# Kernel optimization log

Hardware: AMD Instinct MI355X
Metric: run time of the kernel (lower is better)

## Reference

```python
import jax, jax.numpy as jnp
import numpy as np


def setup_inputs() -> dict:
    key = jax.random.key(0)
    ks = jax.random.split(key, 8)
    b, s1, s2 = 16, 512, 40
    video_dim, text_dim, attn_dim = 1024, 300, 256
    return {
        "video": jax.random.normal(ks[0], (b, s1, video_dim), dtype=jnp.float32),
        "text": jax.random.normal(ks[1], (b, s2, text_dim), dtype=jnp.float32),
        "w1": jax.random.normal(ks[2], (video_dim, attn_dim), dtype=jnp.float32),
        "w2": jax.random.normal(ks[3], (text_dim, attn_dim), dtype=jnp.float32),
        "w3": jax.random.normal(ks[4], (attn_dim, 1), dtype=jnp.float32),
        "bias": jax.random.normal(ks[5], (attn_dim,), dtype=jnp.float32),
        "w4": jax.random.normal(ks[6], (4 * attn_dim, 500), dtype=jnp.float32),
        "b4": jax.random.normal(ks[7], (500,), dtype=jnp.float32),
    }


def reference(video, text, w1, w2, w3, bias, w4, b4):
    # video: (b, s1, d1), text: (b, s2, d2)
    e = jnp.einsum("bsd,da->bsa", video, w1)   # (b, s1, a) -- also 'hh' in original
    f = jnp.einsum("btd,da->bta", text, w2)    # (b, s2, a)
    # additive attention energies: tanh over (b, s1, s2, a) broadcast sum
    h = jnp.tanh(e[:, :, None, :] + f[:, None, :, :] + bias)  # (b, s1, s2, a)
    logits = jnp.squeeze(jnp.einsum("bsta,ao->bsto", h, w3), -1)  # (b, s1, s2)
    # original expands logits over attn_dim then softmaxes dim=2; identical to
    # softmax over s2 of the scalar scores, broadcast afterwards.
    attn = jax.nn.softmax(logits, axis=2)  # (b, s1, s2)
    text_attn = jnp.einsum("bst,bta->bsa", attn, f)  # (b, s1, a)
    cont = jnp.concatenate(
        [e, text_attn, e * text_attn, e - text_attn], axis=-1
    )  # (b, s1, 4a)
    return jnp.tanh(cont) @ w4 + b4  # (b, s1, 500)
```

## Files before the change

### kernel.cpp

```cpp
#include <hip/hip_runtime.h>
#include <hip/hip_bf16.h>
#include <cstdint>

typedef __attribute__((ext_vector_type(8))) short bf16x8;
typedef __attribute__((ext_vector_type(4))) short bf16x4;
typedef __attribute__((ext_vector_type(4))) float f32x4;

#define TANH_SCALE 2.8853900817779268f
#define TANH_UNSCALE 0.34657359027997264f

__device__ __forceinline__ short cvt_bf16(float f) {
  union { float f; uint32_t u; } x; x.f = f;
  uint32_t r = x.u + 0x7FFFu + ((x.u >> 16) & 1u);
  return (short)(r >> 16);
}
__device__ __forceinline__ float bf16_to_f(short s) {
  union { uint32_t u; float f; } x; x.u = ((uint32_t)(uint16_t)s) << 16;
  return x.f;
}

__device__ __forceinline__ float tanh_fast(float x) {
  float e = __builtin_amdgcn_exp2f(x * TANH_SCALE);
  return 1.0f - 2.0f * __builtin_amdgcn_rcpf(e + 1.0f);
}
__device__ __forceinline__ float tanh_pre(float xs) {
  float e = __builtin_amdgcn_exp2f(xs);
  return 1.0f - 2.0f * __builtin_amdgcn_rcpf(e + 1.0f);
}

__global__ __launch_bounds__(256) void k_prep(const float* __restrict__ video,
                                              const float* __restrict__ text,
                                              const float* __restrict__ w1,
                                              const float* __restrict__ w2,
                                              const float* __restrict__ w4,
                                              short* __restrict__ vhi,
                                              short* __restrict__ vlo,
                                              short* __restrict__ w1h,
                                              short* __restrict__ w1l,
                                              short* __restrict__ w4T,
                                              short* __restrict__ th,
                                              short* __restrict__ tl,
                                              short* __restrict__ w2h,
                                              short* __restrict__ w2l) {
  __shared__ float tile[32][33];
  int bid = blockIdx.x;
  if (bid < 1024) {
    int i = bid * 256 + threadIdx.x;
    for (; i < 2097152; i += 1024 * 256) {
      float4 v = ((const float4*)video)[i];
      bf16x4 h, l;
      h.x = cvt_bf16(v.x); h.y = cvt_bf16(v.y); h.z = cvt_bf16(v.z); h.w = cvt_bf16(v.w);
      l.x = cvt_bf16(v.x - bf16_to_f(h.x));
      l.y = cvt_bf16(v.y - bf16_to_f(h.y));
      l.z = cvt_bf16(v.z - bf16_to_f(h.z));
      l.w = cvt_bf16(v.w - bf16_to_f(h.w));
      ((bf16x4*)vhi)[i] = h;
      ((bf16x4*)vlo)[i] = l;
    }
  } else if (bid < 1280) {
    int idx = bid - 1024;
    int r0 = (idx & 31) * 32, c0 = (idx >> 5) * 32;
    int j = threadIdx.x & 31, i0 = threadIdx.x >> 5;
    #pragma unroll
    for (int i = i0; i < 32; i += 8) tile[i][j] = w1[(size_t)(r0 + i) * 256 + c0 + j];
    __syncthreads();
    #pragma unroll
    for (int i = i0; i < 32; i += 8) {
      float v = tile[j][i];
      short h = cvt_bf16(v);
      w1h[(size_t)(c0 + i) * 1024 + r0 + j] = h;
      w1l[(size_t)(c0 + i) * 1024 + r0 + j] = cvt_bf16(v - bf16_to_f(h));
    }
  } else if (bid < 1792) {
    int idx = bid - 1280;
    int r0 = (idx & 31) * 32, c0 = (idx >> 5) * 32;
    int j = threadIdx.x & 31, i0 = threadIdx.x >> 5;
    #pragma unroll
    for (int i = i0; i < 32; i += 8) {
      int c = c0 + j;
      tile[i][j] = (c < 500) ? w4[(size_t)(r0 + i) * 500 + c] : 0.f;
    }
    __syncthreads();
    #pragma unroll
    for (int i = i0; i < 32; i += 8)
      w4T[(size_t)(c0 + i) * 1024 + r0 + j] = cvt_bf16(tile[j][i]);
  } else if (bid < 1952) {
    int idx = bid - 1792;
    int row = idx * 4 + (threadIdx.x >> 6);
    int cl = threadIdx.x & 63;
    const float* trow = text + (size_t)row * 300;
    short* hrow = th + (size_t)row * 320;
    short* lrow = tl + (size_t)row * 320;
    #pragma unroll
    for (int c0 = 0; c0 < 320; c0 += 64) {
      int c = c0 + cl;
      float v = (c < 300) ? trow[c] : 0.f;
      short h = cvt_bf16(v);
      hrow[c] = h;
      lrow[c] = cvt_bf16(v - bf16_to_f(h));
    }
  } else {
    int idx = bid - 1952;
    int rt = idx % 10, ct = idx / 10;
    int r0 = rt * 32, c0 = ct * 32;
    int j = threadIdx.x & 31, i0 = threadIdx.x >> 5;
    #pragma unroll
    for (int i = i0; i < 32; i += 8) {
      int r = r0 + i;
      tile[i][j] = (r < 300) ? w2[(size_t)r * 256 + c0 + j] : 0.f;
    }
    __syncthreads();
    #pragma unroll
    for (int i = i0; i < 32; i += 8) {
      float v = tile[j][i];
      short h = cvt_bf16(v);
      w2h[(size_t)(c0 + i) * 320 + r0 + j] = h;
      w2l[(size_t)(c0 + i) * 320 + r0 + j] = cvt_bf16(v - bf16_to_f(h));
    }
  }
}

__global__ __launch_bounds__(256) void k_gemm_split(const short* __restrict__ Ah,
                                                    const short* __restrict__ Al,
                                                    const short* __restrict__ BTh,
                                                    const short* __restrict__ BTl,
                                                    float* __restrict__ C,
                                                    int K, int ldc) {
  __shared__ __align__(16) short Ash[64][72];
  __shared__ __align__(16) short Asl[64][72];
  __shared__ __align__(16) short Bsh[64][72];
  __shared__ __align__(16) short Bsl[64][72];
  int m0 = blockIdx.x * 64, n0 = blockIdx.y * 64;
  int tid = threadIdx.x, lane = tid & 63, wave = tid >> 6;
  int wm = (wave & 1) * 32, wn = (wave >> 1) * 32;
  int srow = tid >> 3, sseg = (tid & 7) * 8;
  f32x4 acc[2][2];
  #pragma unroll
  for (int i = 0; i < 2; i++)
    #pragma unroll
    for (int j = 0; j < 2; j++) acc[i][j] = (f32x4){0.f, 0.f, 0.f, 0.f};
  int mrow = lane & 15, quad = lane >> 4;

  for (int k0 = 0; k0 < K; k0 += 64) {
    size_t aoff0 = (size_t)(m0 + srow) * K + k0 + sseg;
    size_t aoff1 = aoff0 + (size_t)32 * K;
    size_t boff0 = (size_t)(n0 + srow) * K + k0 + sseg;
    size_t boff1 = boff0 + (size_t)32 * K;
    bf16x8 a0h = *(const bf16x8*)(Ah + aoff0);
    bf16x8 a1h = *(const bf16x8*)(Ah + aoff1);
    bf16x8 a0l = *(const bf16x8*)(Al + aoff0);
    bf16x8 a1l = *(const bf16x8*)(Al + aoff1);
    bf16x8 b0h = *(const bf16x8*)(BTh + boff0);
    bf16x8 b1h = *(const bf16x8*)(BTh + boff1);
    bf16x8 b0l = *(const bf16x8*)(BTl + boff0);
    bf16x8 b1l = *(const bf16x8*)(BTl + boff1);
    __syncthreads();
    *(bf16x8*)&Ash[srow][sseg] = a0h;  *(bf16x8*)&Ash[srow + 32][sseg] = a1h;
    *(bf16x8*)&Asl[srow][sseg] = a0l;  *(bf16x8*)&Asl[srow + 32][sseg] = a1l;
    *(bf16x8*)&Bsh[srow][sseg] = b0h;  *(bf16x8*)&Bsh[srow + 32][sseg] = b1h;
    *(bf16x8*)&Bsl[srow][sseg] = b0l;  *(bf16x8*)&Bsl[srow + 32][sseg] = b1l;
    __syncthreads();
    #pragma unroll
    for (int ks = 0; ks < 2; ks++) {
      int kk = ks * 32 + quad * 8;
      bf16x8 ah[2], al[2], bh[2], bl[2];
      ah[0] = *(const bf16x8*)&Ash[wm + mrow][kk];
      ah[1] = *(const bf16x8*)&Ash[wm + 16 + mrow][kk];
      al[0] = *(const bf16x8*)&Asl[wm + mrow][kk];
      al[1] = *(const bf16x8*)&Asl[wm + 16 + mrow][kk];
      bh[0] = *(const bf16x8*)&Bsh[wn + mrow][kk];
      bh[1] = *(const bf16x8*)&Bsh[wn + 16 + mrow][kk];
      bl[0] = *(const bf16x8*)&Bsl[wn + mrow][kk];
      bl[1] = *(const bf16x8*)&Bsl[wn + 16 + mrow][kk];
      #pragma unroll
      for (int i = 0; i < 2; i++)
        #pragma unroll
        for (int j = 0; j < 2; j++) {
          acc[i][j] = __builtin_amdgcn_mfma_f32_16x16x32_bf16(ah[i], bh[j], acc[i][j], 0, 0, 0);
          acc[i][j] = __builtin_amdgcn_mfma_f32_16x16x32_bf16(ah[i], bl[j], acc[i][j], 0, 0, 0);
          acc[i][j] = __builtin_amdgcn_mfma_f32_16x16x32_bf16(al[i], bh[j], acc[i][j], 0, 0, 0);
        }
    }
  }
  int rbase = quad * 4;
  #pragma unroll
  for (int i = 0; i < 2; i++)
    #pragma unroll
    for (int j = 0; j < 2; j++) {
      int col = n0 + wn + j * 16 + mrow;
      #pragma unroll
      for (int r = 0; r < 4; r++) {
        int row = m0 + wm + i * 16 + rbase + r;
        C[(size_t)row * ldc + col] = acc[i][j][r];
      }
    }
}

__device__ __forceinline__ void load_lds16(void* lds, const void* g) {
  __builtin_amdgcn_global_load_lds(
      (const __attribute__((address_space(1))) void*)g,
      (__attribute__((address_space(3))) void*)lds, 16, 0, 0);
}

__global__ __launch_bounds__(256) void k_gemm_e2(const short* __restrict__ Ah,
                                                 const short* __restrict__ Al,
                                                 const short* __restrict__ BTh,
                                                 const short* __restrict__ BTl,
                                                 float* __restrict__ Cparts,
                                                 int K, int ldc) {
  __shared__ __align__(16) short Ash[128][64];
  __shared__ __align__(16) short Asl[128][64];
  __shared__ __align__(16) short Bsh[64][64];
  __shared__ __align__(16) short Bsl[64][64];
  int m0 = blockIdx.x * 128, n0 = blockIdx.y * 64;
  int kz0 = blockIdx.z * 512;
  int tid = threadIdx.x, lane = tid & 63, wave = tid >> 6;
  int wm = wave * 32;
  int mrow = lane & 15, quad = lane >> 4;
  int lrow = lane >> 3, lseg = (lane & 7) * 8;

  f32x4 acc[2][4];
  #pragma unroll
  for (int i = 0; i < 2; i++)
    #pragma unroll
    for (int j = 0; j < 4; j++) acc[i][j] = (f32x4){0.f, 0.f, 0.f, 0.f};

  for (int k0 = kz0; k0 < kz0 + 512; k0 += 64) {
    __syncthreads();
    #pragma unroll
    for (int i = 0; i < 4; i++) {
      int c = wave * 4 + i;
      size_t go = (size_t)(m0 + c * 8 + lrow) * K + k0 + lseg;
      load_lds16(&Ash[c * 8][0], Ah + go);
      load_lds16(&Asl[c * 8][0], Al + go);
    }
    #pragma unroll
    for (int i = 0; i < 2; i++) {
      int c = wave * 2 + i;
      size_t go = (size_t)(n0 + c * 8 + lrow) * K + k0 + lseg;
      load_lds16(&Bsh[c * 8][0], BTh + go);
      load_lds16(&Bsl[c * 8][0], BTl + go);
    }
    __syncthreads();
    #pragma unroll
    for (int ks = 0; ks < 2; ks++) {
      int kk = ks * 32 + quad * 8;
      bf16x8 ah[2], al[2], bh[4], bl[4];
      #pragma unroll
      for (int i = 0; i < 2; i++) {
        ah[i] = *(const bf16x8*)&Ash[wm + i * 16 + mrow][kk];
        al[i] = *(const bf16x8*)&Asl[wm + i * 16 + mrow][kk];
      }
      #pragma unroll
      for (int j = 0; j < 4; j++) {
        bh[j] = *(const bf16x8*)&Bsh[j * 16 + mrow][kk];
        bl[j] = *(const bf16x8*)&Bsl[j * 16 + mrow][kk];
      }
      #pragma unroll
      for (int i = 0; i < 2; i++)
        #pragma unroll
        for (int j = 0; j < 4; j++) {
          acc[i][j] = __builtin_amdgcn_mfma_f32_16x16x32_bf16(ah[i], bh[j], acc[i][j], 0, 0, 0);
          acc[i][j] = __builtin_amdgcn_mfma_f32_16x16x32_bf16(ah[i], bl[j], acc[i][j], 0, 0, 0);
          acc[i][j] = __builtin_amdgcn_mfma_f32_16x16x32_bf16(al[i], bh[j], acc[i][j], 0, 0, 0);
        }
    }
  }
  float* C = Cparts + (size_t)blockIdx.z * 8192 * 256;
  int rbase = quad * 4;
  #pragma unroll
  for (int i = 0; i < 2; i++)
    #pragma unroll
    for (int j = 0; j < 4; j++) {
      int col = n0 + j * 16 + mrow;
      #pragma unroll
      for (int r = 0; r < 4; r++) {
        int row = m0 + wm + i * 16 + rbase + r;
        C[(size_t)row * ldc + col] = acc[i][j][r];
      }
    }
}

__global__ __launch_bounds__(256) void k_gemm_f(const short* __restrict__ A,
                                                const short* __restrict__ BT,
                                                const float* __restrict__ bias,
                                                float* __restrict__ C,
                                                int K, int ldc, int nstore) {
  __shared__ __align__(16) short As[128][64];
  __shared__ __align__(16) short Bs[64][64];
  int m0 = blockIdx.x * 128, n0 = blockIdx.y * 64;
  int tid = threadIdx.x, lane = tid & 63, wave = tid >> 6;
  int wm = wave * 32;
  int mrow = lane & 15, quad = lane >> 4;
  int lrow = lane >> 3, lseg = (lane & 7) * 8;

  f32x4 acc[2][4];
  #pragma unroll
  for (int i = 0; i < 2; i++)
    #pragma unroll
    for (int j = 0; j < 4; j++) acc[i][j] = (f32x4){0.f, 0.f, 0.f, 0.f};

  for (int k0 = 0; k0 < K; k0 += 64) {
    __syncthreads();
    #pragma unroll
    for (int i = 0; i < 4; i++) {
      int c = wave * 4 + i;
      load_lds16(&As[c * 8][0], A + (size_t)(m0 + c * 8 + lrow) * K + k0 + lseg);
    }
    #pragma unroll
    for (int i = 0; i < 2; i++) {
      int c = wave * 2 + i;
      load_lds16(&Bs[c * 8][0], BT + (size_t)(n0 + c * 8 + lrow) * K + k0 + lseg);
    }
    __syncthreads();
    #pragma unroll
    for (int ks = 0; ks < 2; ks++) {
      int kk = ks * 32 + quad * 8;
      bf16x8 af[2], bf[4];
      #pragma unroll
      for (int i = 0; i < 2; i++) af[i] = *(const bf16x8*)&As[wm + i * 16 + mrow][kk];
      #pragma unroll
      for (int j = 0; j < 4; j++) bf[j] = *(const bf16x8*)&Bs[j * 16 + mrow][kk];
      #pragma unroll
      for (int i = 0; i < 2; i++)
        #pragma unroll
        for (int j = 0; j < 4; j++)
          acc[i][j] = __builtin_amdgcn_mfma_f32_16x16x32_bf16(af[i], bf[j], acc[i][j], 0, 0, 0);
    }
  }
  int rbase = quad * 4;
  #pragma unroll
  for (int i = 0; i < 2; i++)
    #pragma unroll
    for (int j = 0; j < 4; j++) {
      int col = n0 + j * 16 + mrow;
      if (col < nstore) {
        float bv = bias[col];
        #pragma unroll
        for (int r = 0; r < 4; r++) {
          int row = m0 + wm + i * 16 + rbase + r;
          C[(size_t)row * ldc + col] = acc[i][j][r] + bv;
        }
      }
    }
}

__global__ __launch_bounds__(512) void k_middle(const float* __restrict__ e0p,
                                                const float* __restrict__ e1p,
                                                const float* __restrict__ fb,
                                                const float* __restrict__ w3,
                                                const float* __restrict__ bias,
                                                short* __restrict__ cont) {
  __shared__ __align__(16) float fbs[40 * 256];
  __shared__ float lg[16][40];
  __shared__ float attn[16][40];
  int tid = threadIdx.x, wave = tid >> 6, lane = tid & 63;
  int la = lane & 31, half = lane >> 5;
  int row0 = blockIdx.x * 16;
  int b = row0 >> 9;
  int lgrow = wave + (half ? 8 : 0);
  int myrow = row0 + lgrow;

  const float4* fsrc = (const float4*)(fb + (size_t)b * 40 * 256);
  const float4* bias4 = (const float4*)bias;
  for (int i = tid; i < 40 * 64; i += 512) {
    float4 v = fsrc[i];
    float4 bb = bias4[i & 63];
    v.x = (v.x + bb.x) * TANH_SCALE; v.y = (v.y + bb.y) * TANH_SCALE;
    v.z = (v.z + bb.z) * TANH_SCALE; v.w = (v.w + bb.w) * TANH_SCALE;
    ((float4*)fbs)[i] = v;
  }
  __syncthreads();

  int a0 = la * 8;
  size_t eoff = (size_t)myrow * 256 + a0;
  float4 p00 = *(const float4*)(e0p + eoff);
  float4 p01 = *(const float4*)(e0p + eoff + 4);
  float4 p10 = *(const float4*)(e1p + eoff);
  float4 p11 = *(const float4*)(e1p + eoff + 4);
  float4 e0, e1;
  e0.x = p00.x + p10.x; e0.y = p00.y + p10.y; e0.z = p00.z + p10.z; e0.w = p00.w + p10.w;
  e1.x = p01.x + p11.x; e1.y = p01.y + p11.y; e1.z = p01.z + p11.z; e1.w = p01.w + p11.w;
  float4 w30 = *(const float4*)(w3 + a0);
  float4 w31 = *(const float4*)(w3 + a0 + 4);
  float4 bv0 = *(const float4*)(bias + a0);
  float4 bv1 = *(const float4*)(bias + a0 + 4);
  float4 es0, es1;
  es0.x = e0.x * TANH_SCALE; es0.y = e0.y * TANH_SCALE;
  es0.z = e0.z * TANH_SCALE; es0.w = e0.w * TANH_SCALE;
  es1.x = e1.x * TANH_SCALE; es1.y = e1.y * TANH_SCALE;
  es1.z = e1.z * TANH_SCALE; es1.w = e1.w * TANH_SCALE;

  for (int tc = 0; tc < 40; tc += 4) {
    float p[4];
    #pragma unroll
    for (int u = 0; u < 4; u++) {
      const float* fr = &fbs[(tc + u) * 256 + a0];
      float4 f0 = *(const float4*)fr;
      float4 f1 = *(const float4*)(fr + 4);
      p[u] = tanh_pre(es0.x + f0.x) * w30.x + tanh_pre(es0.y + f0.y) * w30.y
           + tanh_pre(es0.z + f0.z) * w30.z + tanh_pre(es0.w + f0.w) * w30.w
           + tanh_pre(es1.x + f1.x) * w31.x + tanh_pre(es1.y + f1.y) * w31.y
           + tanh_pre(es1.z + f1.z) * w31.z + tanh_pre(es1.w + f1.w) * w31.w;
    }
    #pragma unroll
    for (int s = 16; s >= 1; s >>= 1) {
      #pragma unroll
      for (int u = 0; u < 4; u++) p[u] += __shfl_xor(p[u], s, 64);
    }
    if (la == 0) {
      #pragma unroll
      for (int u = 0; u < 4; u++) lg[lgrow][tc + u] = p[u];
    }
  }

  auto softmax_row = [&](int r) {
    float x = (lane < 40) ? lg[r][lane] : -3.0e38f;
    float m = x;
    #pragma unroll
    for (int s = 32; s >= 1; s >>= 1) m = fmaxf(m, __shfl_xor(m, s, 64));
    float ex = (lane < 40) ? __builtin_amdgcn_exp2f((x - m) * 1.4426950408889634f) : 0.f;
    float ssum = ex;
    #pragma unroll
    for (int s = 32; s >= 1; s >>= 1) ssum += __shfl_xor(ssum, s, 64);
    if (lane < 40) attn[r][lane] = ex * __builtin_amdgcn_rcpf(ssum);
  };
  softmax_row(wave);
  softmax_row(wave + 8);

  float ac[8] = {0.f,0.f,0.f,0.f,0.f,0.f,0.f,0.f};
  for (int t = 0; t < 40; t++) {
    float w = attn[lgrow][t];
    const float* fr = &fbs[t * 256 + a0];
    float4 f0 = *(const float4*)fr;
    float4 f1 = *(const float4*)(fr + 4);
    ac[0] += w * f0.x; ac[1] += w * f0.y; ac[2] += w * f0.z; ac[3] += w * f0.w;
    ac[4] += w * f1.x; ac[5] += w * f1.y; ac[6] += w * f1.z; ac[7] += w * f1.w;
  }
  float tx[8];
  tx[0] = ac[0] * TANH_UNSCALE - bv0.x; tx[1] = ac[1] * TANH_UNSCALE - bv0.y;
  tx[2] = ac[2] * TANH_UNSCALE - bv0.z; tx[3] = ac[3] * TANH_UNSCALE - bv0.w;
  tx[4] = ac[4] * TANH_UNSCALE - bv1.x; tx[5] = ac[5] * TANH_UNSCALE - bv1.y;
  tx[6] = ac[6] * TANH_UNSCALE - bv1.z; tx[7] = ac[7] * TANH_UNSCALE - bv1.w;
  float ev[8] = {e0.x, e0.y, e0.z, e0.w, e1.x, e1.y, e1.z, e1.w};

  short* crow = cont + (size_t)myrow * 1024 + a0;
  auto st8 = [&](int off, const float* v) {
    bf16x8 pk;
    #pragma unroll
    for (int i = 0; i < 8; i++) pk[i] = cvt_bf16(v[i]);
    *(bf16x8*)(crow + off) = pk;
  };
  float s0[8], s1[8], s2[8], s3[8];
  #pragma unroll
  for (int i = 0; i < 8; i++) {
    s0[i] = tanh_fast(ev[i]);
    s1[i] = tanh_fast(tx[i]);
    s2[i] = tanh_fast(ev[i] * tx[i]);
    s3[i] = tanh_fast(ev[i] - tx[i]);
  }
  st8(0, s0); st8(256, s1); st8(512, s2); st8(768, s3);
}

extern "C" void kernel_launch(void* const* d_in, const int* in_sizes, int n_in,
                              void* d_out, int out_size, void* d_ws, size_t ws_size,
                              hipStream_t stream) {
  const float* video = (const float*)d_in[0];
  const float* text  = (const float*)d_in[1];
  const float* w1    = (const float*)d_in[2];
  const float* w2    = (const float*)d_in[3];
  const float* w3    = (const float*)d_in[4];
  const float* bias  = (const float*)d_in[5];
  const float* w4    = (const float*)d_in[6];
  const float* b4    = (const float*)d_in[7];
  float* out = (float*)d_out;
  char* ws = (char*)d_ws;

  short* video_hi = (short*)(ws);
  short* video_lo = (short*)(ws + 16777216);
  short* contbuf  = (short*)(ws + 16777216);
  short* w1T_hi   = (short*)(ws + 33554432);
  short* w1T_lo   = (short*)(ws + 34078720);
  short* w4T      = (short*)(ws + 34603008);
  float* fbuf     = (float*)(ws + 35651584);
  float* eparts   = (float*)(ws + 36306944);
  float* epart1   = (float*)(ws + 36306944 + 8388608);
  short* text_hi  = (short*)(ws + 36306944);
  short* text_lo  = (short*)(ws + 36306944 + 409600);
  short* w2T_hi   = (short*)(ws + 36306944 + 819200);
  short* w2T_lo   = (short*)(ws + 36306944 + 1024000);

  k_prep<<<2032, 256, 0, stream>>>(video, text, w1, w2, w4,
                                   video_hi, video_lo, w1T_hi, w1T_lo, w4T,
                                   text_hi, text_lo, w2T_hi, w2T_lo);
  k_gemm_split<<<dim3(10, 4), 256, 0, stream>>>(text_hi, text_lo, w2T_hi, w2T_lo,
                                                fbuf, 320, 256);
  k_gemm_e2<<<dim3(64, 4, 2), 256, 0, stream>>>(video_hi, video_lo, w1T_hi, w1T_lo,
                                                eparts, 1024, 256);
  k_middle<<<512, 512, 0, stream>>>(eparts, epart1, fbuf, w3, bias, contbuf);
  k_gemm_f<<<dim3(64, 8), 256, 0, stream>>>(contbuf, w4T, b4, out, 1024, 500, 500);
}
```

Measured before the change: 174.6 us.

## Fuse video bf16 split into e-GEMM and merge text GEMM into one launch

Result: faster. 164.6 us (-5.7%).

```diff
diff --git a/kernel.cpp b/kernel.cpp
--- a/kernel.cpp
+++ b/kernel.cpp
@@ -23,18 +23,35 @@
   float e = __builtin_amdgcn_exp2f(x * TANH_SCALE);
   return 1.0f - 2.0f * __builtin_amdgcn_rcpf(e + 1.0f);
 }
-__device__ __forceinline__ float tanh_pre(float xs) {
+__device__ __forceinline__ float sig_pre(float xs) {
   float e = __builtin_amdgcn_exp2f(xs);
-  return 1.0f - 2.0f * __builtin_amdgcn_rcpf(e + 1.0f);
-}
-
-__global__ __launch_bounds__(256) void k_prep(const float* __restrict__ video,
-                                              const float* __restrict__ text,
+  return __builtin_amdgcn_rcpf(e + 1.0f);
+}
+
+__device__ __forceinline__ void split8(float4 a, float4 b, bf16x8& h, bf16x8& l) {
+  float fa[8] = {a.x, a.y, a.z, a.w, b.x, b.y, b.z, b.w};
+  uint32_t uh[8], ul[8];
+  #pragma unroll
+  for (int j = 0; j < 8; j++) {
+    union { float f; uint32_t u; } x; x.f = fa[j];
+    uh[j] = x.u;
+    union { uint32_t u; float f; } t; t.u = x.u & 0xffff0000u;
+    union { float f; uint32_t u; } y; y.f = fa[j] - t.f;
+    ul[j] = y.u;
+  }
+  union { uint32_t w[4]; bf16x8 v; } H, L;
+  #pragma unroll
+  for (int j = 0; j < 4; j++) {
+    H.w[j] = __builtin_amdgcn_perm(uh[2 * j + 1], uh[2 * j], 0x07060302u);
+    L.w[j] = __builtin_amdgcn_perm(ul[2 * j + 1], ul[2 * j], 0x07060302u);
+  }
+  h = H.v; l = L.v;
+}
+
+__global__ __launch_bounds__(256) void k_prep(const float* __restrict__ text,
                                               const float* __restrict__ w1,
                                               const float* __restrict__ w2,
                                               const float* __restrict__ w4,
-                                              short* __restrict__ vhi,
-                                              short* __restrict__ vlo,
                                               short* __restrict__ w1h,
                                               short* __restrict__ w1l,
                                               short* __restrict__ w4T,
@@ -44,21 +61,8 @@
                                               short* __restrict__ w2l) {
   __shared__ float tile[32][33];
   int bid = blockIdx.x;
-  if (bid < 1024) {
-    int i = bid * 256 + threadIdx.x;
-    for (; i < 2097152; i += 1024 * 256) {
-      float4 v = ((const float4*)video)[i];
-      bf16x4 h, l;
-      h.x = cvt_bf16(v.x); h.y = cvt_bf16(v.y); h.z = cvt_bf16(v.z); h.w = cvt_bf16(v.w);
-      l.x = cvt_bf16(v.x - bf16_to_f(h.x));
-      l.y = cvt_bf16(v.y - bf16_to_f(h.y));
-      l.z = cvt_bf16(v.z - bf16_to_f(h.z));
-      l.w = cvt_bf16(v.w - bf16_to_f(h.w));
-      ((bf16x4*)vhi)[i] = h;
-      ((bf16x4*)vlo)[i] = l;
-    }
-  } else if (bid < 1280) {
-    int idx = bid - 1024;
+  if (bid < 256) {
+    int idx = bid;
     int r0 = (idx & 31) * 32, c0 = (idx >> 5) * 32;
     int j = threadIdx.x & 31, i0 = threadIdx.x >> 5;
     #pragma unroll
@@ -71,8 +75,8 @@
       w1h[(size_t)(c0 + i) * 1024 + r0 + j] = h;
       w1l[(size_t)(c0 + i) * 1024 + r0 + j] = cvt_bf16(v - bf16_to_f(h));
     }
-  } else if (bid < 1792) {
-    int idx = bid - 1280;
+  } else if (bid < 768) {
+    int idx = bid - 256;
     int r0 = (idx & 31) * 32, c0 = (idx >> 5) * 32;
     int j = threadIdx.x & 31, i0 = threadIdx.x >> 5;
     #pragma unroll
@@ -84,8 +88,8 @@
     #pragma unroll
     for (int i = i0; i < 32; i += 8)
       w4T[(size_t)(c0 + i) * 1024 + r0 + j] = cvt_bf16(tile[j][i]);
-  } else if (bid < 1952) {
-    int idx = bid - 1792;
+  } else if (bid < 928) {
+    int idx = bid - 768;
     int row = idx * 4 + (threadIdx.x >> 6);
     int cl = threadIdx.x & 63;
     const float* trow = text + (size_t)row * 300;
@@ -100,7 +104,7 @@
       lrow[c] = cvt_bf16(v - bf16_to_f(h));
     }
   } else {
-    int idx = bid - 1952;
+    int idx = bid - 928;
     int rt = idx % 10, ct = idx / 10;
     int r0 = rt * 32, c0 = ct * 32;
     int j = threadIdx.x & 31, i0 = threadIdx.x >> 5;
@@ -120,165 +124,186 @@
   }
 }
 
-__global__ __launch_bounds__(256) void k_gemm_split(const short* __restrict__ Ah,
-                                                    const short* __restrict__ Al,
-                                                    const short* __restrict__ BTh,
-                                                    const short* __restrict__ BTl,
-                                                    float* __restrict__ C,
-                                                    int K, int ldc) {
-  __shared__ __align__(16) short Ash[64][72];
-  __shared__ __align__(16) short Asl[64][72];
-  __shared__ __align__(16) short Bsh[64][72];
-  __shared__ __align__(16) short Bsl[64][72];
-  int m0 = blockIdx.x * 64, n0 = blockIdx.y * 64;
-  int tid = threadIdx.x, lane = tid & 63, wave = tid >> 6;
-  int wm = (wave & 1) * 32, wn = (wave >> 1) * 32;
-  int srow = tid >> 3, sseg = (tid & 7) * 8;
-  f32x4 acc[2][2];
-  #pragma unroll
-  for (int i = 0; i < 2; i++)
-    #pragma unroll
-    for (int j = 0; j < 2; j++) acc[i][j] = (f32x4){0.f, 0.f, 0.f, 0.f};
-  int mrow = lane & 15, quad = lane >> 4;
-
-  for (int k0 = 0; k0 < K; k0 += 64) {
-    size_t aoff0 = (size_t)(m0 + srow) * K + k0 + sseg;
-    size_t aoff1 = aoff0 + (size_t)32 * K;
-    size_t boff0 = (size_t)(n0 + srow) * K + k0 + sseg;
-    size_t boff1 = boff0 + (size_t)32 * K;
-    bf16x8 a0h = *(const bf16x8*)(Ah + aoff0);
-    bf16x8 a1h = *(const bf16x8*)(Ah + aoff1);
-    bf16x8 a0l = *(const bf16x8*)(Al + aoff0);
-    bf16x8 a1l = *(const bf16x8*)(Al + aoff1);
-    bf16x8 b0h = *(const bf16x8*)(BTh + boff0);
-    bf16x8 b1h = *(const bf16x8*)(BTh + boff1);
-    bf16x8 b0l = *(const bf16x8*)(BTl + boff0);
-    bf16x8 b1l = *(const bf16x8*)(BTl + boff1);
-    __syncthreads();
-    *(bf16x8*)&Ash[srow][sseg] = a0h;  *(bf16x8*)&Ash[srow + 32][sseg] = a1h;
-    *(bf16x8*)&Asl[srow][sseg] = a0l;  *(bf16x8*)&Asl[srow + 32][sseg] = a1l;
-    *(bf16x8*)&Bsh[srow][sseg] = b0h;  *(bf16x8*)&Bsh[srow + 32][sseg] = b1h;
-    *(bf16x8*)&Bsl[srow][sseg] = b0l;  *(bf16x8*)&Bsl[srow + 32][sseg] = b1l;
-    __syncthreads();
-    #pragma unroll
-    for (int ks = 0; ks < 2; ks++) {
-      int kk = ks * 32 + quad * 8;
-      bf16x8 ah[2], al[2], bh[2], bl[2];
-      ah[0] = *(const bf16x8*)&Ash[wm + mrow][kk];
-      ah[1] = *(const bf16x8*)&Ash[wm + 16 + mrow][kk];
-      al[0] = *(const bf16x8*)&Asl[wm + mrow][kk];
-      al[1] = *(const bf16x8*)&Asl[wm + 16 + mrow][kk];
-      bh[0] = *(const bf16x8*)&Bsh[wn + mrow][kk];
-      bh[1] = *(const bf16x8*)&Bsh[wn + 16 + mrow][kk];
-      bl[0] = *(const bf16x8*)&Bsl[wn + mrow][kk];
-      bl[1] = *(const bf16x8*)&Bsl[wn + 16 + mrow][kk];
-      #pragma unroll
-      for (int i = 0; i < 2; i++)
-        #pragma unroll
-        for (int j = 0; j < 2; j++) {
-          acc[i][j] = __builtin_amdgcn_mfma_f32_16x16x32_bf16(ah[i], bh[j], acc[i][j], 0, 0, 0);
-          acc[i][j] = __builtin_amdgcn_mfma_f32_16x16x32_bf16(ah[i], bl[j], acc[i][j], 0, 0, 0);
-          acc[i][j] = __builtin_amdgcn_mfma_f32_16x16x32_bf16(al[i], bh[j], acc[i][j], 0, 0, 0);
-        }
-    }
-  }
-  int rbase = quad * 4;
-  #pragma unroll
-  for (int i = 0; i < 2; i++)
-    #pragma unroll
-    for (int j = 0; j < 2; j++) {
-      int col = n0 + wn + j * 16 + mrow;
-      #pragma unroll
-      for (int r = 0; r < 4; r++) {
-        int row = m0 + wm + i * 16 + rbase + r;
-        C[(size_t)row * ldc + col] = acc[i][j][r];
-      }
-    }
-}
-
 __device__ __forceinline__ void load_lds16(void* lds, const void* g) {
   __builtin_amdgcn_global_load_lds(
       (const __attribute__((address_space(1))) void*)g,
       (__attribute__((address_space(3))) void*)lds, 16, 0, 0);
 }
 
-__global__ __launch_bounds__(256) void k_gemm_e2(const short* __restrict__ Ah,
-                                                 const short* __restrict__ Al,
-                                                 const short* __restrict__ BTh,
-                                                 const short* __restrict__ BTl,
-                                                 float* __restrict__ Cparts,
-                                                 int K, int ldc) {
-  __shared__ __align__(16) short Ash[128][64];
-  __shared__ __align__(16) short Asl[128][64];
-  __shared__ __align__(16) short Bsh[64][64];
-  __shared__ __align__(16) short Bsl[64][64];
-  int m0 = blockIdx.x * 128, n0 = blockIdx.y * 64;
-  int kz0 = blockIdx.z * 512;
+__global__ __launch_bounds__(256) void k_gemm_big(const float* __restrict__ video,
+                                                  const short* __restrict__ w1h,
+                                                  const short* __restrict__ w1l,
+                                                  const short* __restrict__ th,
+                                                  const short* __restrict__ tl,
+                                                  const short* __restrict__ w2h,
+                                                  const short* __restrict__ w2l,
+                                                  float* __restrict__ eparts,
+                                                  float* __restrict__ fbuf) {
+  __shared__ __align__(16) char smem[49152];
+  int bid = blockIdx.x;
   int tid = threadIdx.x, lane = tid & 63, wave = tid >> 6;
-  int wm = wave * 32;
   int mrow = lane & 15, quad = lane >> 4;
-  int lrow = lane >> 3, lseg = (lane & 7) * 8;
-
-  f32x4 acc[2][4];
-  #pragma unroll
-  for (int i = 0; i < 2; i++)
-    #pragma unroll
-    for (int j = 0; j < 4; j++) acc[i][j] = (f32x4){0.f, 0.f, 0.f, 0.f};
-
-  for (int k0 = kz0; k0 < kz0 + 512; k0 += 64) {
-    __syncthreads();
-    #pragma unroll
-    for (int i = 0; i < 4; i++) {
-      int c = wave * 4 + i;
-      size_t go = (size_t)(m0 + c * 8 + lrow) * K + k0 + lseg;
-      load_lds16(&Ash[c * 8][0], Ah + go);
-      load_lds16(&Asl[c * 8][0], Al + go);
-    }
-    #pragma unroll
-    for (int i = 0; i < 2; i++) {
-      int c = wave * 2 + i;
-      size_t go = (size_t)(n0 + c * 8 + lrow) * K + k0 + lseg;
-      load_lds16(&Bsh[c * 8][0], BTh + go);
-      load_lds16(&Bsl[c * 8][0], BTl + go);
-    }
-    __syncthreads();
-    #pragma unroll
-    for (int ks = 0; ks < 2; ks++) {
-      int kk = ks * 32 + quad * 8;
-      bf16x8 ah[2], al[2], bh[4], bl[4];
+
+  if (bid < 512) {
+    short (*Ash)[64] = (short (*)[64])(smem);
+    short (*Asl)[64] = (short (*)[64])(smem + 16384);
+    short (*Bsh)[64] = (short (*)[64])(smem + 32768);
+    short (*Bsl)[64] = (short (*)[64])(smem + 40960);
+    int m0 = (bid & 63) * 128, n0 = ((bid >> 6) & 3) * 64;
+    int z = bid >> 8;
+    int kz0 = z * 512;
+    int wm = wave * 32;
+    int lrow = lane >> 3, lseg = (lane & 7) * 8;
+
+    f32x4 acc[2][4];
+    #pragma unroll
+    for (int i = 0; i < 2; i++)
+      #pragma unroll
+      for (int j = 0; j < 4; j++) acc[i][j] = (f32x4){0.f, 0.f, 0.f, 0.f};
+
+    float4 va[8];
+    #pragma unroll
+    for (int it = 0; it < 4; it++) {
+      int idx = it * 256 + tid;
+      const float* src = video + (size_t)(m0 + (idx >> 3)) * 1024 + kz0 + (idx & 7) * 8;
+      va[it * 2]     = *(const float4*)src;
+      va[it * 2 + 1] = *(const float4*)(src + 4);
+    }
+
+    for (int k0 = kz0; k0 < kz0 + 512; k0 += 64) {
+      bf16x8 hi[4], lo[4];
+      #pragma unroll
+      for (int it = 0; it < 4; it++) split8(va[it * 2], va[it * 2 + 1], hi[it], lo[it]);
+      __syncthreads();
+      #pragma unroll
+      for (int it = 0; it < 4; it++) {
+        int idx = it * 256 + tid;
+        *(bf16x8*)&Ash[idx >> 3][(idx & 7) * 8] = hi[it];
+        *(bf16x8*)&Asl[idx >> 3][(idx & 7) * 8] = lo[it];
+      }
       #pragma unroll
       for (int i = 0; i < 2; i++) {
-        ah[i] = *(const bf16x8*)&Ash[wm + i * 16 + mrow][kk];
-        al[i] = *(const bf16x8*)&Asl[wm + i * 16 + mrow][kk];
-      }
+        int c = wave * 2 + i;
+        size_t go = (size_t)(n0 + c * 8 + lrow) * 1024 + k0 + lseg;
+        load_lds16(&Bsh[c * 8][0], w1h + go);
+        load_lds16(&Bsl[c * 8][0], w1l + go);
+      }
+      if (k0 + 64 < kz0 + 512) {
+        #pragma unroll
+        for (int it = 0; it < 4; it++) {
+          int idx = it * 256 + tid;
+          const float* src = video + (size_t)(m0 + (idx >> 3)) * 1024 + (k0 + 64) + (idx & 7) * 8;
+          va[it * 2]     = *(const float4*)src;
+          va[it * 2 + 1] = *(const float4*)(src + 4);
+        }
+      }
+      __syncthreads();
+      #pragma unroll
+      for (int ks = 0; ks < 2; ks++) {
+        int kk = ks * 32 + quad * 8;
+        bf16x8 ah[2], al[2], bh[4], bl[4];
+        #pragma unroll
+        for (int i = 0; i < 2; i++) {
+          ah[i] = *(const bf16x8*)&Ash[wm + i * 16 + mrow][kk];
+          al[i] = *(const bf16x8*)&Asl[wm + i * 16 + mrow][kk];
+        }
+        #pragma unroll
+        for (int j = 0; j < 4; j++) {
+          bh[j] = *(const bf16x8*)&Bsh[j * 16 + mrow][kk];
+          bl[j] = *(const bf16x8*)&Bsl[j * 16 + mrow][kk];
+        }
+        #pragma unroll
+        for (int i = 0; i < 2; i++)
+          #pragma unroll
+          for (int j = 0; j < 4; j++) {
+            acc[i][j] = __builtin_amdgcn_mfma_f32_16x16x32_bf16(ah[i], bh[j], acc[i][j], 0, 0, 0);
+            acc[i][j] = __builtin_amdgcn_mfma_f32_16x16x32_bf16(ah[i], bl[j], acc[i][j], 0, 0, 0);
+            acc[i][j] = __builtin_amdgcn_mfma_f32_16x16x32_bf16(al[i], bh[j], acc[i][j], 0, 0, 0);
+          }
+      }
+    }
+    float* C = eparts + (size_t)z * 8192 * 256;
+    int rbase = quad * 4;
+    #pragma unroll
+    for (int i = 0; i < 2; i++)
       #pragma unroll
       for (int j = 0; j < 4; j++) {
-        bh[j] = *(const bf16x8*)&Bsh[j * 16 + mrow][kk];
-        bl[j] = *(const bf16x8*)&Bsl[j * 16 + mrow][kk];
-      }
-      #pragma unroll
-      for (int i = 0; i < 2; i++)
-        #pragma unroll
-        for (int j = 0; j < 4; j++) {
-          acc[i][j] = __builtin_amdgcn_mfma_f32_16x16x32_bf16(ah[i], bh[j], acc[i][j], 0, 0, 0);
-          acc[i][j] = __builtin_amdgcn_mfma_f32_16x16x32_bf16(ah[i], bl[j], acc[i][j], 0, 0, 0);
-          acc[i][j] = __builtin_amdgcn_mfma_f32_16x16x32_bf16(al[i], bh[j], acc[i][j], 0, 0, 0);
+        int col = n0 + j * 16 + mrow;
+        #pragma unroll
+        for (int r = 0; r < 4; r++) {
+          int row = m0 + wm + i * 16 + rbase + r;
+          C[(size_t)row * 256 + col] = acc[i][j][r];
         }
-    }
-  }
-  float* C = Cparts + (size_t)blockIdx.z * 8192 * 256;
-  int rbase = quad * 4;
-  #pragma unroll
-  for (int i = 0; i < 2; i++)
-    #pragma unroll
-    for (int j = 0; j < 4; j++) {
-      int col = n0 + j * 16 + mrow;
-      #pragma unroll
-      for (int r = 0; r < 4; r++) {
-        int row = m0 + wm + i * 16 + rbase + r;
-        C[(size_t)row * ldc + col] = acc[i][j][r];
-      }
-    }
+      }
+  } else {
+    short (*Ash)[72] = (short (*)[72])(smem);
+    short (*Asl)[72] = (short (*)[72])(smem + 9216);
+    short (*Bsh)[72] = (short (*)[72])(smem + 18432);
+    short (*Bsl)[72] = (short (*)[72])(smem + 27648);
+    int idx = bid - 512;
+    int m0 = (idx % 10) * 64, n0 = (idx / 10) * 64;
+    int wm = (wave & 1) * 32, wn = (wave >> 1) * 32;
+    int srow = tid >> 3, sseg = (tid & 7) * 8;
+    f32x4 acc[2][2];
+    #pragma unroll
+    for (int i = 0; i < 2; i++)
+      #pragma unroll
+      for (int j = 0; j < 2; j++) acc[i][j] = (f32x4){0.f, 0.f, 0.f, 0.f};
+
+    for (int k0 = 0; k0 < 320; k0 += 64) {
+      size_t aoff0 = (size_t)(m0 + srow) * 320 + k0 + sseg;
+      size_t aoff1 = aoff0 + (size_t)32 * 320;
+      size_t boff0 = (size_t)(n0 + srow) * 320 + k0 + sseg;
+      size_t boff1 = boff0 + (size_t)32 * 320;
+      bf16x8 a0h = *(const bf16x8*)(th + aoff0);
+      bf16x8 a1h = *(const bf16x8*)(th + aoff1);
+      bf16x8 a0l = *(const bf16x8*)(tl + aoff0);
+      bf16x8 a1l = *(const bf16x8*)(tl + aoff1);
+      bf16x8 b0h = *(const bf16x8*)(w2h + boff0);
+      bf16x8 b1h = *(const bf16x8*)(w2h + boff1);
+      bf16x8 b0l = *(const bf16x8*)(w2l + boff0);
+      bf16x8 b1l = *(const bf16x8*)(w2l + boff1);
+      __syncthreads();
+      *(bf16x8*)&Ash[srow][sseg] = a0h;  *(bf16x8*)&Ash[srow + 32][sseg] = a1h;
+      *(bf16x8*)&Asl[srow][sseg] = a0l;  *(bf16x8*)&Asl[srow + 32][sseg] = a1l;
+      *(bf16x8*)&Bsh[srow][sseg] = b0h;  *(bf16x8*)&Bsh[srow + 32][sseg] = b1h;
+      *(bf16x8*)&Bsl[srow][sseg] = b0l;  *(bf16x8*)&Bsl[srow + 32][sseg] = b1l;
+      __syncthreads();
+      #pragma unroll
+      for (int ks = 0; ks < 2; ks++) {
+        int kk = ks * 32 + quad * 8;
+        bf16x8 ah[2], al[2], bh[2], bl[2];
+        ah[0] = *(const bf16x8*)&Ash[wm + mrow][kk];
+        ah[1] = *(const bf16x8*)&Ash[wm + 16 + mrow][kk];
+        al[0] = *(const bf16x8*)&Asl[wm + mrow][kk];
+        al[1] = *(const bf16x8*)&Asl[wm + 16 + mrow][kk];
+        bh[0] = *(const bf16x8*)&Bsh[wn + mrow][kk];
+        bh[1] = *(const bf16x8*)&Bsh[wn + 16 + mrow][kk];
+        bl[0] = *(const bf16x8*)&Bsl[wn + mrow][kk];
+        bl[1] = *(const bf16x8*)&Bsl[wn + 16 + mrow][kk];
+        #pragma unroll
+        for (int i = 0; i < 2; i++)
+          #pragma unroll
+          for (int j = 0; j < 2; j++) {
+            acc[i][j] = __builtin_amdgcn_mfma_f32_16x16x32_bf16(ah[i], bh[j], acc[i][j], 0, 0, 0);
+            acc[i][j] = __builtin_amdgcn_mfma_f32_16x16x32_bf16(ah[i], bl[j], acc[i][j], 0, 0, 0);
+            acc[i][j] = __builtin_amdgcn_mfma_f32_16x16x32_bf16(al[i], bh[j], acc[i][j], 0, 0, 0);
+          }
+      }
+    }
+    int rbase = quad * 4;
+    #pragma unroll
+    for (int i = 0; i < 2; i++)
+      #pragma unroll
+      for (int j = 0; j < 2; j++) {
+        int col = n0 + wn + j * 16 + mrow;
+        #pragma unroll
+        for (int r = 0; r < 4; r++) {
+          int row = m0 + wm + i * 16 + rbase + r;
+          fbuf[(size_t)row * 256 + col] = acc[i][j][r];
+        }
+      }
+  }
 }
 
 __global__ __launch_bounds__(256) void k_gemm_f(const short* __restrict__ A,
@@ -383,6 +408,8 @@
   e1.x = p01.x + p11.x; e1.y = p01.y + p11.y; e1.z = p01.z + p11.z; e1.w = p01.w + p11.w;
   float4 w30 = *(const float4*)(w3 + a0);
   float4 w31 = *(const float4*)(w3 + a0 + 4);
+  w30.x *= -2.f; w30.y *= -2.f; w30.z *= -2.f; w30.w *= -2.f;
+  w31.x *= -2.f; w31.y *= -2.f; w31.z *= -2.f; w31.w *= -2.f;
   float4 bv0 = *(const float4*)(bias + a0);
   float4 bv1 = *(const float4*)(bias + a0 + 4);
   float4 es0, es1;
@@ -398,10 +425,10 @@
       const float* fr = &fbs[(tc + u) * 256 + a0];
       float4 f0 = *(const float4*)fr;
       float4 f1 = *(const float4*)(fr + 4);
-      p[u] = tanh_pre(es0.x + f0.x) * w30.x + tanh_pre(es0.y + f0.y) * w30.y
-           + tanh_pre(es0.z + f0.z) * w30.z + tanh_pre(es0.w + f0.w) * w30.w
-           + tanh_pre(es1.x + f1.x) * w31.x + tanh_pre(es1.y + f1.y) * w31.y
-           + tanh_pre(es1.z + f1.z) * w31.z + tanh_pre(es1.w + f1.w) * w31.w;
+      p[u] = sig_pre(es0.x + f0.x) * w30.x + sig_pre(es0.y + f0.y) * w30.y
+           + sig_pre(es0.z + f0.z) * w30.z + sig_pre(es0.w + f0.w) * w30.w
+           + sig_pre(es1.x + f1.x) * w31.x + sig_pre(es1.y + f1.y) * w31.y
+           + sig_pre(es1.z + f1.z) * w31.z + sig_pre(es1.w + f1.w) * w31.w;
     }
     #pragma unroll
     for (int s = 16; s >= 1; s >>= 1) {
@@ -476,27 +503,24 @@
   float* out = (float*)d_out;
   char* ws = (char*)d_ws;
 
-  short* video_hi = (short*)(ws);
-  short* video_lo = (short*)(ws + 16777216);
-  short* contbuf  = (short*)(ws + 16777216);
-  short* w1T_hi   = (short*)(ws + 33554432);
-  short* w1T_lo   = (short*)(ws + 34078720);
-  short* w4T      = (short*)(ws + 34603008);
-  float* fbuf     = (float*)(ws + 35651584);
-  float* eparts   = (float*)(ws + 36306944);
-  float* epart1   = (float*)(ws + 36306944 + 8388608);
+  short* contbuf  = (short*)(ws);
+  short* w1T_hi   = (short*)(ws + 16777216);
+  short* w1T_lo   = (short*)(ws + 17301504);
+  short* w4T      = (short*)(ws + 17825792);
+  float* fbuf     = (float*)(ws + 18874368);
+  float* eparts   = (float*)(ws + 19529728);
+  float* epart1   = (float*)(ws + 19529728 + 8388608);
   short* text_hi  = (short*)(ws + 36306944);
-  short* text_lo  = (short*)(ws + 36306944 + 409600);
-  short* w2T_hi   = (short*)(ws + 36306944 + 819200);
-  short* w2T_lo   = (short*)(ws + 36306944 + 1024000);
-
-  k_prep<<<2032, 256, 0, stream>>>(video, text, w1, w2, w4,
-                                   video_hi, video_lo, w1T_hi, w1T_lo, w4T,
+  short* text_lo  = (short*)(ws + 36716544);
+  short* w2T_hi   = (short*)(ws + 37126144);
+  short* w2T_lo   = (short*)(ws + 37330944);
+
+  k_prep<<<1008, 256, 0, stream>>>(text, w1, w2, w4,
+                                   w1T_hi, w1T_lo, w4T,
                                    text_hi, text_lo, w2T_hi, w2T_lo);
-  k_gemm_split<<<dim3(10, 4), 256, 0, stream>>>(text_hi, text_lo, w2T_hi, w2T_lo,
-                                                fbuf, 320, 256);
-  k_gemm_e2<<<dim3(64, 4, 2), 256, 0, stream>>>(video_hi, video_lo, w1T_hi, w1T_lo,
-                                                eparts, 1024, 256);
+  k_gemm_big<<<552, 256, 0, stream>>>(video, w1T_hi, w1T_lo,
+                                      text_hi, text_lo, w2T_hi, w2T_lo,
+                                      eparts, fbuf);
   k_middle<<<512, 512, 0, stream>>>(eparts, epart1, fbuf, w3, bias, contbuf);
   k_gemm_f<<<dim3(64, 8), 256, 0, stream>>>(contbuf, w4T, b4, out, 1024, 500, 500);
 }
```
